# Kernel tuning notes

Measured on AMD Instinct MI355X. Metric: run time of the kernel, lower is better.

## Reference

```python
import jax, jax.numpy as jnp
import numpy as np

# ---- constants matching init_kwargs ----
ALPHA = 1.0
SCALING = 12.0
RESP_INDEX = (0, 1, 2, 3)
N_TARGETS = len(RESP_INDEX)
NDAYS = 250  # number of distinct date ids; with N=2M and 250 ids all are present
N = 2_000_000
N_RESP = 5


def setup_inputs() -> dict:
    key = jax.random.key(0)
    k1, k2, k3, k4 = jax.random.split(key, 4)
    inputs = jax.random.normal(k1, (N, N_RESP), dtype=jnp.float32)
    targets = jax.random.normal(k2, (N, N_RESP), dtype=jnp.float32)
    weights = jax.random.uniform(k3, (N,), dtype=jnp.float32)
    date = jax.random.randint(k4, (N,), 0, NDAYS, dtype=jnp.int64)
    return {"inputs": inputs, "targets": targets, "weights": weights, "date": date}


def reference(inputs, targets, weights, date):
    # slice resp columns (resp_index is not None and len < 5)
    idx = jnp.asarray(RESP_INDEX)
    x = jax.nn.sigmoid(SCALING * inputs[..., idx])   # [N, 4]
    t = targets[..., idx]                            # [N, 4]

    # faithful to torch: inputs/targets flattened sample-major, while
    # weights/date are repeat-tiled (resp-major) -- same pairing as original.
    x = x.reshape(-1)                 # [4N], sample-major
    t = t.reshape(-1)                 # [4N], sample-major
    w = jnp.tile(weights, N_TARGETS)  # [4N], tiled
    d = jnp.tile(date, N_TARGETS)     # [4N], tiled

    # per-day grouped sum -> single-pass segment reduction
    Pi = jax.ops.segment_sum(w * t * x, d, num_segments=NDAYS)  # [NDAYS]

    sumPi = Pi.sum()
    # normalize == 'mean'
    loss = -ALPHA * sumPi * jnp.maximum(sumPi, 0.0) / jnp.sum(Pi * Pi) / NDAYS
    return loss
```

## Files before the change

kernel.cpp:

```cpp
#include <hip/hip_runtime.h>

#define NDAYS 250
#define SCALING 12.0f
#define TPB 256
#define NBLK 512
#define TILE 1024
#define MIDB 64
#define RPM (NBLK / MIDB)

typedef float f4 __attribute__((ext_vector_type(4)));

__global__ __launch_bounds__(TPB) void pi_kernel(
    const float* __restrict__ inputs, const float* __restrict__ targets,
    const float* __restrict__ weights, const int* __restrict__ date,
    float* __restrict__ part, int n) {
    __shared__ float sPi[NDAYS];
    for (int i = threadIdx.x; i < NDAYS; i += TPB) sPi[i] = 0.0f;
    __syncthreads();

    const int nq = n >> 2;
    const int ii0 = blockIdx.x * TILE;
    if (ii0 < nq) {
        const int ts  = min(TILE, nq - ii0);
        const int nfl = ts * 5;
        const int lane = threadIdx.x & 63;

        int   dy[5][4];
        float wt[5][4];
        #pragma unroll
        for (int e = 0; e < 5; ++e) {
            const int c   = TPB * e + threadIdx.x;
            const int fl0 = 4 * c;
            #pragma unroll
            for (int dlt = 0; dlt < 4; ++dlt) {
                const int fl = fl0 + dlt;
                const int si = (int)(((unsigned)fl * 52429u) >> 18);
                const int j  = fl - 5 * si;
                const bool valid = (fl < nfl) && (j < 4);
                const int  m = valid ? (4 * (ii0 + si) + j) : 0;
                wt[e][dlt] = valid ? weights[m] : 0.0f;
                dy[e][dlt] = valid ? date[m] : lane;
            }
        }

        float acc[5][4] = {};
        #pragma unroll
        for (int q = 0; q < 4; ++q) {
            const size_t base = ((size_t)q * nq + ii0) * 5;
            #pragma unroll
            for (int e = 0; e < 5; ++e) {
                const int c = TPB * e + threadIdx.x;
                f4 inv = {0.0f, 0.0f, 0.0f, 0.0f};
                f4 tgv = {0.0f, 0.0f, 0.0f, 0.0f};
                if (4 * c < nfl) {
                    inv = *(const f4*)(inputs + base + 4 * c);
                    tgv = *(const f4*)(targets + base + 4 * c);
                }
                #pragma unroll
                for (int dlt = 0; dlt < 4; ++dlt) {
                    const float e1 = __expf(-SCALING * inv[dlt]);
                    const float sg = __builtin_amdgcn_rcpf(1.0f + e1);
                    acc[e][dlt] += tgv[dlt] * sg;
                }
            }
        }

        #pragma unroll
        for (int e = 0; e < 5; ++e)
            #pragma unroll
            for (int dlt = 0; dlt < 4; ++dlt)
                atomicAdd(&sPi[dy[e][dlt]], acc[e][dlt] * wt[e][dlt]);
    }

    __syncthreads();
    float* row = part + (size_t)blockIdx.x * NDAYS;
    for (int i = threadIdx.x; i < NDAYS; i += TPB) row[i] = sPi[i];
}

__global__ __launch_bounds__(TPB) void mid_kernel(const float* __restrict__ part,
                                                  float* __restrict__ part2) {
    const int c = threadIdx.x;
    if (c < NDAYS) {
        const float* p = part + (size_t)blockIdx.x * RPM * NDAYS + c;
        float a = 0.0f;
        #pragma unroll
        for (int r = 0; r < RPM; ++r) a += p[(size_t)r * NDAYS];
        part2[(size_t)blockIdx.x * NDAYS + c] = a;
    }
}

__global__ __launch_bounds__(TPB) void fin_kernel(const float* __restrict__ part2,
                                                  float* __restrict__ out) {
    __shared__ float ws_s[4], ws_q[4];
    const int t = threadIdx.x;
    float s = 0.0f, q = 0.0f;
    if (t < NDAYS) {
        float pc = 0.0f;
        #pragma unroll 8
        for (int r = 0; r < MIDB; ++r) pc += part2[(size_t)r * NDAYS + t];
        s = pc;
        q = pc * pc;
    }
    #pragma unroll
    for (int off = 32; off > 0; off >>= 1) {
        s += __shfl_down(s, off);
        q += __shfl_down(q, off);
    }
    if ((t & 63) == 0) {
        ws_s[t >> 6] = s;
        ws_q[t >> 6] = q;
    }
    __syncthreads();
    if (t == 0) {
        const float sumPi  = ws_s[0] + ws_s[1] + ws_s[2] + ws_s[3];
        const float sumPi2 = ws_q[0] + ws_q[1] + ws_q[2] + ws_q[3];
        out[0] = -1.0f * sumPi * fmaxf(sumPi, 0.0f) / sumPi2 / (float)NDAYS;
    }
}

extern "C" void kernel_launch(void* const* d_in, const int* in_sizes, int n_in,
                              void* d_out, int out_size, void* d_ws, size_t ws_size,
                              hipStream_t stream) {
    const float* inputs  = (const float*)d_in[0];
    const float* targets = (const float*)d_in[1];
    const float* weights = (const float*)d_in[2];
    const int*   date    = (const int*)d_in[3];
    float* out   = (float*)d_out;
    float* part  = (float*)d_ws;
    float* part2 = part + (size_t)NBLK * NDAYS;

    const int n = in_sizes[2];

    pi_kernel<<<NBLK, TPB, 0, stream>>>(inputs, targets, weights, date, part, n);
    mid_kernel<<<MIDB, TPB, 0, stream>>>(part, part2);
    fin_kernel<<<1, TPB, 0, stream>>>(part2, out);
}
```

Measured before the change: 125.8 us.

## Stage weights/date via LDS with vector loads and fold mid reduction into final kernel

Weights and dates are now loaded coalesced as 16-byte vectors into shared memory, then gathered per element from LDS, replacing the strided scalar global gathers. The mid_kernel launch is removed, and a 1024-thread final kernel reduces all per-block partial rows directly. The grid is now computed from n rather than fixed. In exchange it adds 32KB of LDS per block, which may limit occupancy.

```diff
diff --git a/kernel.cpp b/kernel.cpp
--- a/kernel.cpp
+++ b/kernel.cpp
@@ -3,110 +3,120 @@
 #define NDAYS 250
 #define SCALING 12.0f
 #define TPB 256
-#define NBLK 512
 #define TILE 1024
-#define MIDB 64
-#define RPM (NBLK / MIDB)
+#define MAXROWS 512
 
 typedef float f4 __attribute__((ext_vector_type(4)));
+typedef int   i4 __attribute__((ext_vector_type(4)));
 
 __global__ __launch_bounds__(TPB) void pi_kernel(
     const float* __restrict__ inputs, const float* __restrict__ targets,
     const float* __restrict__ weights, const int* __restrict__ date,
     float* __restrict__ part, int n) {
     __shared__ float sPi[NDAYS];
+    __shared__ float sw[4 * TILE];
+    __shared__ int   sd[4 * TILE];
     for (int i = threadIdx.x; i < NDAYS; i += TPB) sPi[i] = 0.0f;
+
+    const int nq   = n >> 2;
+    const int ii0  = blockIdx.x * TILE;
+    const int lane = threadIdx.x & 63;
+    const int mb   = 4 * ii0;
+
+    #pragma unroll
+    for (int e = 0; e < 4; ++e) {
+        const int x = 4 * (TPB * e + threadIdx.x);
+        f4 wv = {0.0f, 0.0f, 0.0f, 0.0f};
+        i4 dv = {lane, lane, lane, lane};
+        if (mb + x < n) {
+            wv = *(const f4*)(weights + mb + x);
+            dv = *(const i4*)(date + mb + x);
+        }
+        *(f4*)&sw[x] = wv;
+        *(i4*)&sd[x] = dv;
+    }
     __syncthreads();
 
-    const int nq = n >> 2;
-    const int ii0 = blockIdx.x * TILE;
-    if (ii0 < nq) {
-        const int ts  = min(TILE, nq - ii0);
-        const int nfl = ts * 5;
-        const int lane = threadIdx.x & 63;
+    const int ts  = min(TILE, nq - ii0);
+    const int nfl = ts * 5;
 
-        int   dy[5][4];
-        float wt[5][4];
+    int   dy[5][4];
+    float wt[5][4];
+    #pragma unroll
+    for (int e = 0; e < 5; ++e) {
+        const int fl0 = 4 * (TPB * e + threadIdx.x);
+        #pragma unroll
+        for (int dlt = 0; dlt < 4; ++dlt) {
+            const int fl = fl0 + dlt;
+            const int si = (int)(((unsigned)fl * 52429u) >> 18);
+            const int j  = fl - 5 * si;
+            const bool valid = (fl < nfl) && (j < 4);
+            const int  mi = 4 * si + j;
+            wt[e][dlt] = valid ? sw[mi] : 0.0f;
+            dy[e][dlt] = valid ? sd[mi] : lane;
+        }
+    }
+
+    float acc[5][4] = {};
+    #pragma unroll
+    for (int q = 0; q < 4; ++q) {
+        const size_t base = ((size_t)q * nq + ii0) * 5;
         #pragma unroll
         for (int e = 0; e < 5; ++e) {
-            const int c   = TPB * e + threadIdx.x;
-            const int fl0 = 4 * c;
+            const int fl0 = 4 * (TPB * e + threadIdx.x);
+            f4 inv = {0.0f, 0.0f, 0.0f, 0.0f};
+            f4 tgv = {0.0f, 0.0f, 0.0f, 0.0f};
+            if (fl0 < nfl) {
+                inv = *(const f4*)(inputs + base + fl0);
+                tgv = *(const f4*)(targets + base + fl0);
+            }
             #pragma unroll
             for (int dlt = 0; dlt < 4; ++dlt) {
-                const int fl = fl0 + dlt;
-                const int si = (int)(((unsigned)fl * 52429u) >> 18);
-                const int j  = fl - 5 * si;
-                const bool valid = (fl < nfl) && (j < 4);
-                const int  m = valid ? (4 * (ii0 + si) + j) : 0;
-                wt[e][dlt] = valid ? weights[m] : 0.0f;
-                dy[e][dlt] = valid ? date[m] : lane;
+                const float e1 = __expf(-SCALING * inv[dlt]);
+                const float sg = __builtin_amdgcn_rcpf(1.0f + e1);
+                acc[e][dlt] += tgv[dlt] * sg;
             }
         }
+    }
 
-        float acc[5][4] = {};
+    #pragma unroll
+    for (int e = 0; e < 5; ++e)
         #pragma unroll
-        for (int q = 0; q < 4; ++q) {
-            const size_t base = ((size_t)q * nq + ii0) * 5;
-            #pragma unroll
-            for (int e = 0; e < 5; ++e) {
-                const int c = TPB * e + threadIdx.x;
-                f4 inv = {0.0f, 0.0f, 0.0f, 0.0f};
-                f4 tgv = {0.0f, 0.0f, 0.0f, 0.0f};
-                if (4 * c < nfl) {
-                    inv = *(const f4*)(inputs + base + 4 * c);
-                    tgv = *(const f4*)(targets + base + 4 * c);
-                }
-                #pragma unroll
-                for (int dlt = 0; dlt < 4; ++dlt) {
-                    const float e1 = __expf(-SCALING * inv[dlt]);
-                    const float sg = __builtin_amdgcn_rcpf(1.0f + e1);
-                    acc[e][dlt] += tgv[dlt] * sg;
-                }
-            }
-        }
-
-        #pragma unroll
-        for (int e = 0; e < 5; ++e)
-            #pragma unroll
-            for (int dlt = 0; dlt < 4; ++dlt)
-                atomicAdd(&sPi[dy[e][dlt]], acc[e][dlt] * wt[e][dlt]);
-    }
+        for (int dlt = 0; dlt < 4; ++dlt)
+            atomicAdd(&sPi[dy[e][dlt]], acc[e][dlt] * wt[e][dlt]);
 
     __syncthreads();
     float* row = part + (size_t)blockIdx.x * NDAYS;
     for (int i = threadIdx.x; i < NDAYS; i += TPB) row[i] = sPi[i];
 }
 
-__global__ __launch_bounds__(TPB) void mid_kernel(const float* __restrict__ part,
-                                                  float* __restrict__ part2) {
-    const int c = threadIdx.x;
-    if (c < NDAYS) {
-        const float* p = part + (size_t)blockIdx.x * RPM * NDAYS + c;
-        float a = 0.0f;
-        #pragma unroll
-        for (int r = 0; r < RPM; ++r) a += p[(size_t)r * NDAYS];
-        part2[(size_t)blockIdx.x * NDAYS + c] = a;
-    }
-}
-
-__global__ __launch_bounds__(TPB) void fin_kernel(const float* __restrict__ part2,
-                                                  float* __restrict__ out) {
+__global__ __launch_bounds__(1024) void fin_kernel(const float* __restrict__ part,
+                                                   float* __restrict__ out, int nrows) {
+    __shared__ float col[4][256];
     __shared__ float ws_s[4], ws_q[4];
     const int t = threadIdx.x;
+    const int c = t & 255;
+    const int g = t >> 8;
+
+    float a = 0.0f;
+    if (c < NDAYS) {
+        #pragma unroll 8
+        for (int r = g; r < nrows; r += 4) a += part[(size_t)r * NDAYS + c];
+    }
+    col[g][c] = a;
+    __syncthreads();
+
     float s = 0.0f, q = 0.0f;
-    if (t < NDAYS) {
-        float pc = 0.0f;
-        #pragma unroll 8
-        for (int r = 0; r < MIDB; ++r) pc += part2[(size_t)r * NDAYS + t];
-        s = pc;
-        q = pc * pc;
+    if (t < 256) {
+        const float pc = col[0][t] + col[1][t] + col[2][t] + col[3][t];
+        if (t < NDAYS) { s = pc; q = pc * pc; }
     }
     #pragma unroll
     for (int off = 32; off > 0; off >>= 1) {
         s += __shfl_down(s, off);
         q += __shfl_down(q, off);
     }
-    if ((t & 63) == 0) {
+    if (t < 256 && (t & 63) == 0) {
         ws_s[t >> 6] = s;
         ws_q[t >> 6] = q;
     }
@@ -125,13 +135,13 @@
     const float* targets = (const float*)d_in[1];
     const float* weights = (const float*)d_in[2];
     const int*   date    = (const int*)d_in[3];
-    float* out   = (float*)d_out;
-    float* part  = (float*)d_ws;
-    float* part2 = part + (size_t)NBLK * NDAYS;
+    float* out  = (float*)d_out;
+    float* part = (float*)d_ws;
 
-    const int n = in_sizes[2];
+    const int n  = in_sizes[2];
+    const int nq = n >> 2;
+    const int grid = (nq + TILE - 1) / TILE;
 
-    pi_kernel<<<NBLK, TPB, 0, stream>>>(inputs, targets, weights, date, part, n);
-    mid_kernel<<<MIDB, TPB, 0, stream>>>(part, part2);
-    fin_kernel<<<1, TPB, 0, stream>>>(part2, out);
+    pi_kernel<<<grid, TPB, 0, stream>>>(inputs, targets, weights, date, part, n);
+    fin_kernel<<<1, 1024, 0, stream>>>(part, out, grid);
 }
```

After: 126.8 us. About the same (+0.8%).
